# Kernel tuning notes

Measured on AMD Instinct MI355X. Metric: run time of the kernel, lower is better.

Reference implementation:

```python
import jax, jax.numpy as jnp
import numpy as np

B, T, H = 65536, 24, 64  # batch, input_window_size, num_neurons
SLOPE = 25.0             # snntorch fast_sigmoid default slope

@jax.custom_vjp
def spike(x):
    # heaviside forward, fast-sigmoid surrogate backward
    return (x > 0).astype(x.dtype)

def _spike_fwd(x):
    return (x > 0).astype(x.dtype), x

def _spike_bwd(x, g):
    return (g / (SLOPE * jnp.abs(x) + 1.0) ** 2,)

spike.defvjp(_spike_fwd, _spike_bwd)

def slstm_cell(x, syn, mem, Wih, Whh, bih, bhh, thr):
    # snntorch SLSTM: LSTMCell with h=mem, c=syn; reset_mechanism='subtract'
    reset = jax.lax.stop_gradient((mem - thr > 0).astype(x.dtype))
    gates = x @ Wih.T + bih + mem @ Whh.T + bhh  # (B, 4H)
    i, f, g, o = jnp.split(gates, 4, axis=-1)
    syn_new = jax.nn.sigmoid(f) * syn + jax.nn.sigmoid(i) * jnp.tanh(g)
    mem_new = jax.nn.sigmoid(o) * jnp.tanh(syn_new) - reset * thr
    spk = spike(mem_new - thr)
    return spk, syn_new, mem_new

def setup_inputs() -> dict:
    key = jax.random.key(0)
    ks = jax.random.split(key, 11)
    s = float(1.0 / np.sqrt(H))  # LSTMCell uniform init bound
    so = float(1.0 / np.sqrt((T + 2) * H))
    u = lambda k, shape: jax.random.uniform(k, shape, jnp.float32, -s, s)
    return {
        "x": jax.random.normal(ks[0], (B, T, 1), jnp.float32),
        "Wih1": u(ks[1], (4 * H, 1)),
        "Whh1": u(ks[2], (4 * H, H)),
        "bih1": u(ks[3], (4 * H,)),
        "bhh1": u(ks[4], (4 * H,)),
        "thr1": jnp.float32(0.5),
        "Wih2": u(ks[5], (4 * H, H)),
        "Whh2": u(ks[6], (4 * H, H)),
        "bih2": u(ks[7], (4 * H,)),
        "bhh2": u(ks[8], (4 * H,)),
        "thr2": jnp.float32(0.5),
        "Wout": jax.random.uniform(ks[9], (2, (T + 2) * H), jnp.float32, -so, so),
        "bout": jnp.array([0.2, -0.2], jnp.float32),
    }

def reference(x, Wih1, Whh1, bih1, bhh1, thr1,
              Wih2, Whh2, bih2, bhh2, thr2, Wout, bout):
    Bn = x.shape[0]
    Hn = Whh1.shape[1]
    z = jnp.zeros((Bn, Hn), x.dtype)
    carry0 = (z, z, z, z)  # syn1, mem1, syn2, mem2

    def step(carry, xt):
        syn1, mem1, syn2, mem2 = carry
        spk1, syn1, mem1 = slstm_cell(xt, syn1, mem1, Wih1, Whh1, bih1, bhh1, thr1)
        spk2, syn2, mem2 = slstm_cell(spk1, syn2, mem2, Wih2, Whh2, bih2, bhh2, thr2)
        return (syn1, mem1, syn2, mem2), spk2

    (syn1, mem1, syn2, mem2), spk2_seq = jax.lax.scan(
        step, carry0, jnp.swapaxes(x, 0, 1))  # spk2_seq: (T, B, H)
    # extra step: feed mem1 into slstm2
    spk2_last, syn2, mem2 = slstm_cell(mem1, syn2, mem2, Wih2, Whh2, bih2, bhh2, thr2)
    lst = jnp.concatenate(
        [jnp.swapaxes(spk2_seq, 0, 1).reshape(Bn, -1), spk2_last, mem2], axis=1)
    return lst @ Wout.T + bout  # (B, 2)
```

## Files before the change

### kernel.cpp

```cpp
#include <hip/hip_runtime.h>
#include <cstdint>
#include <cstddef>


#define BB 65536
#define TT 24
#define NB 8

__device__ __forceinline__ float bcastf(float v, int l) {
  return __int_as_float(__builtin_amdgcn_readlane(__float_as_int(v), l));
}
__device__ __forceinline__ float sigm(float v) {
  return __fdividef(1.0f, 1.0f + __expf(-v));
}
__device__ __forceinline__ float tanh_fast(float v) {
  return fmaf(-2.0f, __fdividef(1.0f, __expf(2.0f * v) + 1.0f), 1.0f);
}
__device__ __forceinline__ float wsum(float v) {
#pragma unroll
  for (int o = 32; o > 0; o >>= 1) v += __shfl_xor(v, o);
  return v;
}

__global__ __attribute__((amdgpu_waves_per_eu(4, 4))) __launch_bounds__(512)
void snn_pass1(
    const float* __restrict__ x, const float* __restrict__ Wih1,
    const float* __restrict__ Whh1, const float* __restrict__ bih1,
    const float* __restrict__ bhh1, const float* __restrict__ thr1p,
    unsigned long long* __restrict__ spk_out, float* __restrict__ mem1_out) {
  __shared__ float4 P1[64][64];
  __shared__ float stM[8][64][NB];
  int tid = threadIdx.x;
  for (int idx = tid; idx < 16384; idx += 512) {
    int k = idx >> 6, m = idx & 63;
    ((float*)&P1[m][k & 63])[k >> 6] = Whh1[idx];
  }
  __syncthreads();
  int lane = tid & 63, wave = tid >> 6;
  int wb = (blockIdx.x * 8 + wave) * NB;
  float thr1 = thr1p[0];
  float b1q[4], wq[4];
#pragma unroll
  for (int q = 0; q < 4; q++) {
    b1q[q] = bih1[q * 64 + lane] + bhh1[q * 64 + lane];
    wq[q] = Wih1[q * 64 + lane];
  }
  float syn[NB], mem[NB];
#pragma unroll
  for (int b = 0; b < NB; b++) { syn[b] = 0.0f; mem[b] = 0.0f; }

  for (int t = 0; t < TT; t++) {
#pragma unroll
    for (int b = 0; b < NB; b++) stM[wave][lane][b] = mem[b];
    unsigned long long myspk = 0;
#pragma unroll
    for (int h = 0; h < 2; h++) {
      const int B0 = h * 4;
      float acc[4][4];
#pragma unroll
      for (int j = 0; j < 4; j++) {
        float xbt = x[(wb + B0 + j) * TT + t];
#pragma unroll
        for (int q = 0; q < 4; q++) acc[j][q] = fmaf(xbt, wq[q], b1q[q]);
      }
#pragma unroll 8
      for (int m = 0; m < 64; m++) {
        float4 w = P1[m][lane];
        float4 sa = *(const float4*)&stM[wave][m][B0];
        float s[4] = {sa.x, sa.y, sa.z, sa.w};
#pragma unroll
        for (int j = 0; j < 4; j++) {
          acc[j][0] = fmaf(s[j], w.x, acc[j][0]);
          acc[j][1] = fmaf(s[j], w.y, acc[j][1]);
          acc[j][2] = fmaf(s[j], w.z, acc[j][2]);
          acc[j][3] = fmaf(s[j], w.w, acc[j][3]);
        }
      }
#pragma unroll
      for (int j = 0; j < 4; j++) {
        int b = B0 + j;
        float ig = sigm(acc[j][0]), fg = sigm(acc[j][1]);
        float gg = tanh_fast(acc[j][2]), og = sigm(acc[j][3]);
        float sn = fmaf(fg, syn[b], ig * gg);
        float rst = (mem[b] > thr1) ? thr1 : 0.0f;
        float mn = fmaf(og, tanh_fast(sn), -rst);
        syn[b] = sn;
        mem[b] = mn;
        unsigned long long msk = __ballot(mn > thr1);
        if (lane == b) myspk = msk;
      }
      __builtin_amdgcn_sched_barrier(0);
    }
    if (lane < NB)
      spk_out[(size_t)t * BB + wb + lane] = myspk;
  }
#pragma unroll
  for (int b = 0; b < NB; b++)
    mem1_out[(size_t)(wb + b) * 64 + lane] = mem[b];
}

__global__ __attribute__((amdgpu_waves_per_eu(4, 4))) __launch_bounds__(1024)
void snn_pass2(
    const float* __restrict__ Wih2, const float* __restrict__ Whh2,
    const float* __restrict__ bih2, const float* __restrict__ bhh2,
    const float* __restrict__ thr2p, const float* __restrict__ Wout,
    const float* __restrict__ bout,
    const unsigned long long* __restrict__ spk_in,
    const float* __restrict__ mem1_in, float* __restrict__ out) {
  __shared__ float4 Pih[64][64];
  __shared__ float4 Phh[64][64];
  __shared__ float stM[16][64][NB];
  int tid = threadIdx.x;
  for (int idx = tid; idx < 16384; idx += 1024) {
    int k = idx >> 6, m = idx & 63;
    ((float*)&Pih[m][k & 63])[k >> 6] = Wih2[idx];
    ((float*)&Phh[m][k & 63])[k >> 6] = Whh2[idx];
  }
  __syncthreads();
  int lane = tid & 63, wave = tid >> 6;
  int wb = (blockIdx.x * 16 + wave) * NB;
  float thr2 = thr2p[0];
  float b2q[4];
#pragma unroll
  for (int q = 0; q < 4; q++) b2q[q] = bih2[q * 64 + lane] + bhh2[q * 64 + lane];
  float syn[NB], mem[NB];
  unsigned sb8[NB];
#pragma unroll
  for (int b = 0; b < NB; b++) { syn[b] = 0.0f; mem[b] = 0.0f; sb8[b] = 0u; }

  for (int t = 0; t < TT; t++) {
    unsigned long long mk[NB];
#pragma unroll
    for (int b = 0; b < NB; b++) {
      unsigned long long v = spk_in[(size_t)t * BB + wb + b];
      unsigned lo = __builtin_amdgcn_readfirstlane((unsigned)v);
      unsigned hi = __builtin_amdgcn_readfirstlane((unsigned)(v >> 32));
      mk[b] = ((unsigned long long)hi << 32) | (unsigned long long)lo;
    }
#pragma unroll
    for (int b = 0; b < NB; b++) stM[wave][lane][b] = mem[b];
#pragma unroll
    for (int h = 0; h < 2; h++) {
      const int B0 = h * 4;
      float acc[4][4];
#pragma unroll
      for (int j = 0; j < 4; j++) {
#pragma unroll
        for (int q = 0; q < 4; q++) acc[j][q] = b2q[q];
      }
#pragma unroll 4
      for (int m = 0; m < 64; m++) {
        float4 wh = Phh[m][lane];
        float4 sa = *(const float4*)&stM[wave][m][B0];
        float s[4] = {sa.x, sa.y, sa.z, sa.w};
#pragma unroll
        for (int j = 0; j < 4; j++) {
          acc[j][0] = fmaf(s[j], wh.x, acc[j][0]);
          acc[j][1] = fmaf(s[j], wh.y, acc[j][1]);
          acc[j][2] = fmaf(s[j], wh.z, acc[j][2]);
          acc[j][3] = fmaf(s[j], wh.w, acc[j][3]);
        }
      }
#pragma unroll
      for (int j = 0; j < 4; j++) {
        int b = B0 + j;
        unsigned long long k = mk[b];
        while (__builtin_popcountll(k) >= 4) {
          int m0 = __builtin_ctzll(k); k &= k - 1;
          int m1 = __builtin_ctzll(k); k &= k - 1;
          int m2 = __builtin_ctzll(k); k &= k - 1;
          int m3 = __builtin_ctzll(k); k &= k - 1;
          float4 r0 = Pih[m0][lane];
          float4 r1 = Pih[m1][lane];
          float4 r2 = Pih[m2][lane];
          float4 r3 = Pih[m3][lane];
          acc[j][0] += r0.x; acc[j][1] += r0.y; acc[j][2] += r0.z; acc[j][3] += r0.w;
          acc[j][0] += r1.x; acc[j][1] += r1.y; acc[j][2] += r1.z; acc[j][3] += r1.w;
          acc[j][0] += r2.x; acc[j][1] += r2.y; acc[j][2] += r2.z; acc[j][3] += r2.w;
          acc[j][0] += r3.x; acc[j][1] += r3.y; acc[j][2] += r3.z; acc[j][3] += r3.w;
        }
        while (k) {
          int m0 = __builtin_ctzll(k); k &= k - 1;
          float4 r0 = Pih[m0][lane];
          acc[j][0] += r0.x; acc[j][1] += r0.y; acc[j][2] += r0.z; acc[j][3] += r0.w;
        }
        float ig = sigm(acc[j][0]), fg = sigm(acc[j][1]);
        float gg = tanh_fast(acc[j][2]), og = sigm(acc[j][3]);
        float sn = fmaf(fg, syn[b], ig * gg);
        float rst = (mem[b] > thr2) ? thr2 : 0.0f;
        float mn = fmaf(og, tanh_fast(sn), -rst);
        syn[b] = sn;
        mem[b] = mn;
        sb8[b] |= (mn > thr2) ? (1u << t) : 0u;
      }
      __builtin_amdgcn_sched_barrier(0);
    }
  }

  float m1[NB];
#pragma unroll
  for (int b = 0; b < NB; b++) m1[b] = mem1_in[(size_t)(wb + b) * 64 + lane];
  float acc[NB][4];
#pragma unroll
  for (int b = 0; b < NB; b++) {
#pragma unroll
    for (int q = 0; q < 4; q++) acc[b][q] = b2q[q];
  }
#pragma unroll 4
  for (int m = 0; m < 64; m++) {
    float4 wi = Pih[m][lane];
    float4 wh = Phh[m][lane];
#pragma unroll
    for (int b = 0; b < NB; b++) {
      float s1 = bcastf(m1[b], m);
      float s2 = bcastf(mem[b], m);
      acc[b][0] = fmaf(s1, wi.x, fmaf(s2, wh.x, acc[b][0]));
      acc[b][1] = fmaf(s1, wi.y, fmaf(s2, wh.y, acc[b][1]));
      acc[b][2] = fmaf(s1, wi.z, fmaf(s2, wh.z, acc[b][2]));
      acc[b][3] = fmaf(s1, wi.w, fmaf(s2, wh.w, acc[b][3]));
    }
  }
  float p0[NB], p1[NB];
#pragma unroll
  for (int b = 0; b < NB; b++) { p0[b] = 0.0f; p1[b] = 0.0f; }
#pragma unroll 4
  for (int t = 0; t < TT; t++) {
    float w0 = Wout[t * 64 + lane];
    float w1 = Wout[1664 + t * 64 + lane];
#pragma unroll
    for (int b = 0; b < NB; b++) {
      float sf = ((sb8[b] >> t) & 1u) ? 1.0f : 0.0f;
      p0[b] = fmaf(sf, w0, p0[b]);
      p1[b] = fmaf(sf, w1, p1[b]);
    }
  }
  float wA0 = Wout[1536 + lane], wA1 = Wout[1664 + 1536 + lane];
  float wB0 = Wout[1600 + lane], wB1 = Wout[1664 + 1600 + lane];
  float bo0 = bout[0], bo1 = bout[1];
#pragma unroll
  for (int b = 0; b < NB; b++) {
    float ig = sigm(acc[b][0]), fg = sigm(acc[b][1]);
    float gg = tanh_fast(acc[b][2]), og = sigm(acc[b][3]);
    float sn = fmaf(fg, syn[b], ig * gg);
    float rst = (mem[b] > thr2) ? thr2 : 0.0f;
    float mn = fmaf(og, tanh_fast(sn), -rst);
    float sf = (mn > thr2) ? 1.0f : 0.0f;
    p0[b] = fmaf(sf, wA0, p0[b]);
    p1[b] = fmaf(sf, wA1, p1[b]);
    p0[b] = fmaf(mn, wB0, p0[b]);
    p1[b] = fmaf(mn, wB1, p1[b]);
  }
  float vout = 0.0f;
#pragma unroll
  for (int b = 0; b < NB; b++) {
    float r0 = wsum(p0[b]);
    float r1 = wsum(p1[b]);
    if (lane == 2 * b) vout = r0;
    if (lane == 2 * b + 1) vout = r1;
  }
  if (lane < 2 * NB)
    out[(size_t)wb * 2 + lane] = vout + ((lane & 1) ? bo1 : bo0);
}

extern "C" void kernel_launch(void* const* d_in, const int* in_sizes, int n_in,
                              void* d_out, int out_size, void* d_ws, size_t ws_size,
                              hipStream_t stream) {
  const float* x = (const float*)d_in[0];
  const float* Wih1 = (const float*)d_in[1];
  const float* Whh1 = (const float*)d_in[2];
  const float* bih1 = (const float*)d_in[3];
  const float* bhh1 = (const float*)d_in[4];
  const float* thr1 = (const float*)d_in[5];
  const float* Wih2 = (const float*)d_in[6];
  const float* Whh2 = (const float*)d_in[7];
  const float* bih2 = (const float*)d_in[8];
  const float* bhh2 = (const float*)d_in[9];
  const float* thr2 = (const float*)d_in[10];
  const float* Wout = (const float*)d_in[11];
  const float* bout = (const float*)d_in[12];

  unsigned long long* spk = (unsigned long long*)d_ws;
  float* mem1 = (float*)((char*)d_ws + (size_t)TT * BB * 8);

  snn_pass1<<<BB / (8 * NB), 512, 0, stream>>>(x, Wih1, Whh1, bih1, bhh1, thr1,
                                               spk, mem1);
  snn_pass2<<<BB / (16 * NB), 1024, 0, stream>>>(Wih2, Whh2, bih2, bhh2, thr2,
                                                 Wout, bout, spk, mem1,
                                                 (float*)d_out);
}
```

Baseline: 1.756 ms.

## Double per-wave batch tile to 16 and stream layer-2 spikes through workspace

```diff
diff --git a/kernel.cpp b/kernel.cpp
--- a/kernel.cpp
+++ b/kernel.cpp
@@ -5,7 +5,7 @@
 
 #define BB 65536
 #define TT 24
-#define NB 8
+#define NB 16
 
 __device__ __forceinline__ float bcastf(float v, int l) {
   return __int_as_float(__builtin_amdgcn_readlane(__float_as_int(v), l));
@@ -22,7 +22,7 @@
   return v;
 }
 
-__global__ __attribute__((amdgpu_waves_per_eu(4, 4))) __launch_bounds__(512)
+__global__ __attribute__((amdgpu_waves_per_eu(2, 4))) __launch_bounds__(512)
 void snn_pass1(
     const float* __restrict__ x, const float* __restrict__ Wih1,
     const float* __restrict__ Whh1, const float* __restrict__ bih1,
@@ -55,10 +55,10 @@
     unsigned long long myspk = 0;
 #pragma unroll
     for (int h = 0; h < 2; h++) {
-      const int B0 = h * 4;
-      float acc[4][4];
-#pragma unroll
-      for (int j = 0; j < 4; j++) {
+      const int B0 = h * 8;
+      float acc[8][4];
+#pragma unroll
+      for (int j = 0; j < 8; j++) {
         float xbt = x[(wb + B0 + j) * TT + t];
 #pragma unroll
         for (int q = 0; q < 4; q++) acc[j][q] = fmaf(xbt, wq[q], b1q[q]);
@@ -67,9 +67,10 @@
       for (int m = 0; m < 64; m++) {
         float4 w = P1[m][lane];
         float4 sa = *(const float4*)&stM[wave][m][B0];
-        float s[4] = {sa.x, sa.y, sa.z, sa.w};
-#pragma unroll
-        for (int j = 0; j < 4; j++) {
+        float4 sb4 = *(const float4*)&stM[wave][m][B0 + 4];
+        float s[8] = {sa.x, sa.y, sa.z, sa.w, sb4.x, sb4.y, sb4.z, sb4.w};
+#pragma unroll
+        for (int j = 0; j < 8; j++) {
           acc[j][0] = fmaf(s[j], w.x, acc[j][0]);
           acc[j][1] = fmaf(s[j], w.y, acc[j][1]);
           acc[j][2] = fmaf(s[j], w.z, acc[j][2]);
@@ -77,7 +78,7 @@
         }
       }
 #pragma unroll
-      for (int j = 0; j < 4; j++) {
+      for (int j = 0; j < 8; j++) {
         int b = B0 + j;
         float ig = sigm(acc[j][0]), fg = sigm(acc[j][1]);
         float gg = tanh_fast(acc[j][2]), og = sigm(acc[j][3]);
@@ -99,52 +100,52 @@
     mem1_out[(size_t)(wb + b) * 64 + lane] = mem[b];
 }
 
-__global__ __attribute__((amdgpu_waves_per_eu(4, 4))) __launch_bounds__(1024)
+__global__ __attribute__((amdgpu_waves_per_eu(2, 4))) __launch_bounds__(512)
 void snn_pass2(
     const float* __restrict__ Wih2, const float* __restrict__ Whh2,
     const float* __restrict__ bih2, const float* __restrict__ bhh2,
     const float* __restrict__ thr2p, const float* __restrict__ Wout,
     const float* __restrict__ bout,
-    const unsigned long long* __restrict__ spk_in,
+    unsigned long long* __restrict__ spk_io,
     const float* __restrict__ mem1_in, float* __restrict__ out) {
   __shared__ float4 Pih[64][64];
   __shared__ float4 Phh[64][64];
-  __shared__ float stM[16][64][NB];
+  __shared__ float stM[8][64][NB];
   int tid = threadIdx.x;
-  for (int idx = tid; idx < 16384; idx += 1024) {
+  for (int idx = tid; idx < 16384; idx += 512) {
     int k = idx >> 6, m = idx & 63;
     ((float*)&Pih[m][k & 63])[k >> 6] = Wih2[idx];
     ((float*)&Phh[m][k & 63])[k >> 6] = Whh2[idx];
   }
   __syncthreads();
   int lane = tid & 63, wave = tid >> 6;
-  int wb = (blockIdx.x * 16 + wave) * NB;
+  int wb = (blockIdx.x * 8 + wave) * NB;
   float thr2 = thr2p[0];
   float b2q[4];
 #pragma unroll
   for (int q = 0; q < 4; q++) b2q[q] = bih2[q * 64 + lane] + bhh2[q * 64 + lane];
   float syn[NB], mem[NB];
-  unsigned sb8[NB];
-#pragma unroll
-  for (int b = 0; b < NB; b++) { syn[b] = 0.0f; mem[b] = 0.0f; sb8[b] = 0u; }
+#pragma unroll
+  for (int b = 0; b < NB; b++) { syn[b] = 0.0f; mem[b] = 0.0f; }
 
   for (int t = 0; t < TT; t++) {
     unsigned long long mk[NB];
 #pragma unroll
     for (int b = 0; b < NB; b++) {
-      unsigned long long v = spk_in[(size_t)t * BB + wb + b];
+      unsigned long long v = spk_io[(size_t)t * BB + wb + b];
       unsigned lo = __builtin_amdgcn_readfirstlane((unsigned)v);
       unsigned hi = __builtin_amdgcn_readfirstlane((unsigned)(v >> 32));
       mk[b] = ((unsigned long long)hi << 32) | (unsigned long long)lo;
     }
 #pragma unroll
     for (int b = 0; b < NB; b++) stM[wave][lane][b] = mem[b];
+    unsigned long long myspk2 = 0;
 #pragma unroll
     for (int h = 0; h < 2; h++) {
-      const int B0 = h * 4;
-      float acc[4][4];
-#pragma unroll
-      for (int j = 0; j < 4; j++) {
+      const int B0 = h * 8;
+      float acc[8][4];
+#pragma unroll
+      for (int j = 0; j < 8; j++) {
 #pragma unroll
         for (int q = 0; q < 4; q++) acc[j][q] = b2q[q];
       }
@@ -152,9 +153,10 @@
       for (int m = 0; m < 64; m++) {
         float4 wh = Phh[m][lane];
         float4 sa = *(const float4*)&stM[wave][m][B0];
-        float s[4] = {sa.x, sa.y, sa.z, sa.w};
-#pragma unroll
-        for (int j = 0; j < 4; j++) {
+        float4 sb4 = *(const float4*)&stM[wave][m][B0 + 4];
+        float s[8] = {sa.x, sa.y, sa.z, sa.w, sb4.x, sb4.y, sb4.z, sb4.w};
+#pragma unroll
+        for (int j = 0; j < 8; j++) {
           acc[j][0] = fmaf(s[j], wh.x, acc[j][0]);
           acc[j][1] = fmaf(s[j], wh.y, acc[j][1]);
           acc[j][2] = fmaf(s[j], wh.z, acc[j][2]);
@@ -162,7 +164,7 @@
         }
       }
 #pragma unroll
-      for (int j = 0; j < 4; j++) {
+      for (int j = 0; j < 8; j++) {
         int b = B0 + j;
         unsigned long long k = mk[b];
         while (__builtin_popcountll(k) >= 4) {
@@ -191,70 +193,82 @@
         float mn = fmaf(og, tanh_fast(sn), -rst);
         syn[b] = sn;
         mem[b] = mn;
-        sb8[b] |= (mn > thr2) ? (1u << t) : 0u;
+        unsigned long long msk2 = __ballot(mn > thr2);
+        if (lane == b) myspk2 = msk2;
       }
       __builtin_amdgcn_sched_barrier(0);
     }
-  }
-
-  float m1[NB];
-#pragma unroll
-  for (int b = 0; b < NB; b++) m1[b] = mem1_in[(size_t)(wb + b) * 64 + lane];
-  float acc[NB][4];
-#pragma unroll
+    if (lane < NB)
+      spk_io[(size_t)t * BB + wb + lane] = myspk2;
+  }
+
+  float mnx[NB];
+  unsigned sfx = 0u;
+#pragma unroll
+  for (int h = 0; h < 2; h++) {
+    const int B0 = h * 8;
+    float m1[8];
+#pragma unroll
+    for (int j = 0; j < 8; j++) m1[j] = mem1_in[(size_t)(wb + B0 + j) * 64 + lane];
+    float acc[8][4];
+#pragma unroll
+    for (int j = 0; j < 8; j++) {
+#pragma unroll
+      for (int q = 0; q < 4; q++) acc[j][q] = b2q[q];
+    }
+#pragma unroll 4
+    for (int m = 0; m < 64; m++) {
+      float4 wi = Pih[m][lane];
+      float4 wh = Phh[m][lane];
+#pragma unroll
+      for (int j = 0; j < 8; j++) {
+        float s1 = bcastf(m1[j], m);
+        float s2 = bcastf(mem[B0 + j], m);
+        acc[j][0] = fmaf(s1, wi.x, fmaf(s2, wh.x, acc[j][0]));
+        acc[j][1] = fmaf(s1, wi.y, fmaf(s2, wh.y, acc[j][1]));
+        acc[j][2] = fmaf(s1, wi.z, fmaf(s2, wh.z, acc[j][2]));
+        acc[j][3] = fmaf(s1, wi.w, fmaf(s2, wh.w, acc[j][3]));
+      }
+    }
+#pragma unroll
+    for (int j = 0; j < 8; j++) {
+      int b = B0 + j;
+      float ig = sigm(acc[j][0]), fg = sigm(acc[j][1]);
+      float gg = tanh_fast(acc[j][2]), og = sigm(acc[j][3]);
+      float sn = fmaf(fg, syn[b], ig * gg);
+      float rst = (mem[b] > thr2) ? thr2 : 0.0f;
+      float mn = fmaf(og, tanh_fast(sn), -rst);
+      mnx[b] = mn;
+      sfx |= (mn > thr2) ? (1u << b) : 0u;
+    }
+    __builtin_amdgcn_sched_barrier(0);
+  }
+
+  __threadfence();
+  float bo0 = bout[0], bo1 = bout[1];
+  float vout = 0.0f;
+#pragma unroll 2
   for (int b = 0; b < NB; b++) {
-#pragma unroll
-    for (int q = 0; q < 4; q++) acc[b][q] = b2q[q];
-  }
+    unsigned long long mv = 0ull;
+    if (lane < TT) mv = spk_io[(size_t)lane * BB + wb + b];
+    unsigned vlo = (unsigned)mv, vhi = (unsigned)(mv >> 32);
+    float p0b = 0.0f, p1b = 0.0f;
 #pragma unroll 4
-  for (int m = 0; m < 64; m++) {
-    float4 wi = Pih[m][lane];
-    float4 wh = Phh[m][lane];
-#pragma unroll
-    for (int b = 0; b < NB; b++) {
-      float s1 = bcastf(m1[b], m);
-      float s2 = bcastf(mem[b], m);
-      acc[b][0] = fmaf(s1, wi.x, fmaf(s2, wh.x, acc[b][0]));
-      acc[b][1] = fmaf(s1, wi.y, fmaf(s2, wh.y, acc[b][1]));
-      acc[b][2] = fmaf(s1, wi.z, fmaf(s2, wh.z, acc[b][2]));
-      acc[b][3] = fmaf(s1, wi.w, fmaf(s2, wh.w, acc[b][3]));
-    }
-  }
-  float p0[NB], p1[NB];
-#pragma unroll
-  for (int b = 0; b < NB; b++) { p0[b] = 0.0f; p1[b] = 0.0f; }
-#pragma unroll 4
-  for (int t = 0; t < TT; t++) {
-    float w0 = Wout[t * 64 + lane];
-    float w1 = Wout[1664 + t * 64 + lane];
-#pragma unroll
-    for (int b = 0; b < NB; b++) {
-      float sf = ((sb8[b] >> t) & 1u) ? 1.0f : 0.0f;
-      p0[b] = fmaf(sf, w0, p0[b]);
-      p1[b] = fmaf(sf, w1, p1[b]);
-    }
-  }
-  float wA0 = Wout[1536 + lane], wA1 = Wout[1664 + 1536 + lane];
-  float wB0 = Wout[1600 + lane], wB1 = Wout[1664 + 1600 + lane];
-  float bo0 = bout[0], bo1 = bout[1];
-#pragma unroll
-  for (int b = 0; b < NB; b++) {
-    float ig = sigm(acc[b][0]), fg = sigm(acc[b][1]);
-    float gg = tanh_fast(acc[b][2]), og = sigm(acc[b][3]);
-    float sn = fmaf(fg, syn[b], ig * gg);
-    float rst = (mem[b] > thr2) ? thr2 : 0.0f;
-    float mn = fmaf(og, tanh_fast(sn), -rst);
-    float sf = (mn > thr2) ? 1.0f : 0.0f;
-    p0[b] = fmaf(sf, wA0, p0[b]);
-    p1[b] = fmaf(sf, wA1, p1[b]);
-    p0[b] = fmaf(mn, wB0, p0[b]);
-    p1[b] = fmaf(mn, wB1, p1[b]);
-  }
-  float vout = 0.0f;
-#pragma unroll
-  for (int b = 0; b < NB; b++) {
-    float r0 = wsum(p0[b]);
-    float r1 = wsum(p1[b]);
+    for (int t = 0; t < TT; t++) {
+      unsigned lo = (unsigned)__builtin_amdgcn_readlane((int)vlo, t);
+      unsigned hi = (unsigned)__builtin_amdgcn_readlane((int)vhi, t);
+      unsigned long long mt = ((unsigned long long)hi << 32) | (unsigned long long)lo;
+      float sf = ((mt >> lane) & 1ull) ? 1.0f : 0.0f;
+      p0b = fmaf(sf, Wout[t * 64 + lane], p0b);
+      p1b = fmaf(sf, Wout[1664 + t * 64 + lane], p1b);
+    }
+    float sfb = ((sfx >> b) & 1u) ? 1.0f : 0.0f;
+    p0b = fmaf(sfb, Wout[1536 + lane], p0b);
+    p1b = fmaf(sfb, Wout[1664 + 1536 + lane], p1b);
+    p0b = fmaf(mnx[b], Wout[1600 + lane], p0b);
+    p1b = fmaf(mnx[b], Wout[1664 + 1600 + lane], p1b);
+    float r0 = wsum(p0b);
+    float r1 = wsum(p1b);
     if (lane == 2 * b) vout = r0;
     if (lane == 2 * b + 1) vout = r1;
   }
@@ -282,9 +296,8 @@
   unsigned long long* spk = (unsigned long long*)d_ws;
   float* mem1 = (float*)((char*)d_ws + (size_t)TT * BB * 8);
 
-  snn_pass1<<<BB / (8 * NB), 512, 0, stream>>>(x, Wih1, Whh1, bih1, bhh1, thr1,
-                                               spk, mem1);
-  snn_pass2<<<BB / (16 * NB), 1024, 0, stream>>>(Wih2, Whh2, bih2, bhh2, thr2,
-                                                 Wout, bout, spk, mem1,
-                                                 (float*)d_out);
-}
+  const int grid = BB / (8 * NB);
+  snn_pass1<<<grid, 512, 0, stream>>>(x, Wih1, Whh1, bih1, bhh1, thr1, spk, mem1);
+  snn_pass2<<<grid, 512, 0, stream>>>(Wih2, Whh2, bih2, bhh2, thr2, Wout, bout,
+                                      spk, mem1, (float*)d_out);
+}
```

Result: slower. 1.919 ms (+9.3%).
